# Optimization experiments

Hardware: AMD Instinct MI355X
Metric: run time of the kernel (lower is better)

The kernel has to match this reference:

```python
import jax, jax.numpy as jnp
import numpy as np

B, S, D = 2, 2048, 1024
H, DK, DV = 16, 64, 64

def setup_inputs() -> dict:
    key = jax.random.key(0)
    ks = jax.random.split(key, 5)
    scale = 1.0 / np.sqrt(D)  # xavier-ish
    return {
        "Q": jax.random.normal(ks[0], (B, S, D), dtype=jnp.float32),
        "attn_mask": jax.random.uniform(ks[1], (B, S), dtype=jnp.float32),
        "W_Q": jax.random.normal(ks[2], (H * DK, D), dtype=jnp.float32) * scale,
        "b_Q": jnp.zeros((H * DK,), dtype=jnp.float32),
        "W_K": jax.random.normal(ks[3], (H * DK, D), dtype=jnp.float32) * scale,
        "b_K": jnp.zeros((H * DK,), dtype=jnp.float32),
        "W_V": jax.random.normal(ks[4], (H * DV, D), dtype=jnp.float32) * scale,
        "b_V": jnp.zeros((H * DV,), dtype=jnp.float32),
    }

def reference(Q, attn_mask, W_Q, b_Q, W_K, b_K, W_V, b_V):
    b, s, _ = Q.shape
    # projections -> [B, H, S, d]
    q = (Q @ W_Q.T + b_Q).reshape(b, s, H, DK).transpose(0, 2, 1, 3)
    k = (Q @ W_K.T + b_K).reshape(b, s, H, DK).transpose(0, 2, 1, 3)
    v = (Q @ W_V.T + b_V).reshape(b, s, H, DV).transpose(0, 2, 1, 3)
    # exp-based attention (NOT stable softmax), multiplicative mask
    scores = jnp.einsum('bhqd,bhkd->bhqk', q, k) / np.sqrt(DK)
    scores = jnp.exp(scores)
    # mask [B, S_key] broadcast over heads and queries -> [B, 1, 1, S]
    scores = scores * attn_mask[:, None, None, :]
    attn = scores / (jnp.sum(scores, axis=-1, keepdims=True) + 1e-8)
    context = jnp.einsum('bhqk,bhkd->bhqd', attn, v)
    # [B, H, S, DV] -> [B, S, H*DV]
    return context.transpose(0, 2, 1, 3).reshape(b, s, H * DV)
```

## Files before the change

### kernel.cpp

```cpp
#include <hip/hip_runtime.h>
#include <hip/hip_bf16.h>
#include <math.h>

#define BATCH  2
#define S_LEN  2048
#define DMODEL 1024
#define NH     16
#define DHEAD  64

typedef __attribute__((ext_vector_type(8))) short bf16x8;
typedef __attribute__((ext_vector_type(4))) float f32x4;

#define MFMA16(a,b,c) __builtin_amdgcn_mfma_f32_16x16x32_bf16((a),(b),(c),0,0,0)

__device__ __forceinline__ unsigned int pkbf(float a, float b) {
    __hip_bfloat162 h = __float22bfloat162_rn(make_float2(a, b));
    union { __hip_bfloat162 h; unsigned int u; } v; v.h = h; return v.u;
}
__device__ __forceinline__ void gl2lds16(const void* g, void* l) {
    __builtin_amdgcn_global_load_lds(
        (const __attribute__((address_space(1))) void*)(g),
        (__attribute__((address_space(3))) void*)(l), 16, 0, 0);
}

__global__ __launch_bounds__(256) void cvt_bf16(
    const float* __restrict__ src, unsigned short* __restrict__ dst, int n8)
{
    int i = blockIdx.x * blockDim.x + threadIdx.x;
    if (i >= n8) return;
    float4 a = ((const float4*)src)[2*i];
    float4 b = ((const float4*)src)[2*i + 1];
    uint4 o;
    o.x = pkbf(a.x, a.y); o.y = pkbf(a.z, a.w);
    o.z = pkbf(b.x, b.y); o.w = pkbf(b.z, b.w);
    ((uint4*)dst)[i] = o;
}

__global__ __launch_bounds__(256) void proj_mfma(
    const unsigned short* __restrict__ Abf,
    const unsigned short* __restrict__ Wbf,
    const float* __restrict__ bQ, const float* __restrict__ bK,
    const float* __restrict__ bV, const float* __restrict__ mask,
    unsigned short* __restrict__ qw, unsigned short* __restrict__ kw,
    unsigned short* __restrict__ vt)
{
    __shared__ union {
        struct { unsigned short At[128*32]; unsigned short Bt[128*32]; } s;
        unsigned short Ct[128*132];
    } sm;

    const int tid  = threadIdx.x;
    const int lane = tid & 63;
    const int wv   = tid >> 6;
    const int wm   = (wv >> 1) * 64;
    const int wn   = (wv & 1) * 64;
    const int q15  = lane & 15;
    const int quad = lane >> 4;
    const int z    = blockIdx.z;
    const int n0   = blockIdx.x * 128;
    const int m0   = blockIdx.y * 128;

    const unsigned short* Wz = Wbf + (size_t)z * DMODEL * DMODEL;
    const float* bias = (z == 0) ? bQ : ((z == 1) ? bK : bV);

    f32x4 zero4 = {0.f, 0.f, 0.f, 0.f};
    f32x4 acc[4][4];
    #pragma unroll
    for (int i = 0; i < 4; ++i)
        #pragma unroll
        for (int j = 0; j < 4; ++j) acc[i][j] = zero4;

    for (int k0 = 0; k0 < DMODEL; k0 += 32) {
        __syncthreads();
        #pragma unroll
        for (int c = 0; c < 2; ++c) {
            int o   = tid * 16 + c * 4096;
            int row = o >> 6;
            int cb  = o & 63;
            gl2lds16(Abf + (size_t)(m0 + row) * DMODEL + k0 + (cb >> 1),
                     (char*)sm.s.At + o);
            gl2lds16(Wz  + (size_t)(n0 + row) * DMODEL + k0 + (cb >> 1),
                     (char*)sm.s.Bt + o);
        }
        __syncthreads();

        bf16x8 af[4], bf[4];
        #pragma unroll
        for (int i = 0; i < 4; ++i)
            af[i] = *(const bf16x8*)(sm.s.At + (wm + i*16 + q15) * 32 + quad * 8);
        #pragma unroll
        for (int j = 0; j < 4; ++j)
            bf[j] = *(const bf16x8*)(sm.s.Bt + (wn + j*16 + q15) * 32 + quad * 8);

        if (z < 2) {
            #pragma unroll
            for (int i = 0; i < 4; ++i)
                #pragma unroll
                for (int j = 0; j < 4; ++j)
                    acc[i][j] = MFMA16(bf[j], af[i], acc[i][j]);
        } else {
            #pragma unroll
            for (int i = 0; i < 4; ++i)
                #pragma unroll
                for (int j = 0; j < 4; ++j)
                    acc[i][j] = MFMA16(af[i], bf[j], acc[i][j]);
        }
    }

    __syncthreads();

    if (z < 2) {
        const float qs = (z == 0) ? 0.125f : 1.0f;
        #pragma unroll
        for (int i = 0; i < 4; ++i) {
            int ml = wm + i*16 + q15;
            #pragma unroll
            for (int j = 0; j < 4; ++j) {
                int nl = wn + j*16 + quad*4;
                float4 b4 = *(const float4*)(bias + n0 + nl);
                f32x4 v = acc[i][j];
                uint2 u;
                u.x = pkbf((v.x + b4.x)*qs, (v.y + b4.y)*qs);
                u.y = pkbf((v.z + b4.z)*qs, (v.w + b4.w)*qs);
                *(uint2*)&sm.Ct[ml*132 + nl] = u;
            }
        }
    } else {
        #pragma unroll
        for (int i = 0; i < 4; ++i) {
            int ml = wm + i*16 + quad*4;
            int sg = m0 + ml;
            int b2 = sg >> 11, s0g = sg & 2047;
            float4 mk4 = *(const float4*)(mask + (size_t)b2*S_LEN + s0g);
            #pragma unroll
            for (int j = 0; j < 4; ++j) {
                int nl = wn + j*16 + q15;
                float bv = bias[n0 + nl];
                f32x4 v = acc[i][j];
                uint2 u;
                u.x = pkbf((v.x + bv)*mk4.x, (v.y + bv)*mk4.y);
                u.y = pkbf((v.z + bv)*mk4.z, (v.w + bv)*mk4.w);
                *(uint2*)&sm.Ct[nl*132 + ml] = u;
            }
        }
    }
    __syncthreads();

    {
        int row  = tid >> 1;
        int half = (tid & 1) * 64;
        const uint4* src = (const uint4*)&sm.Ct[row*132 + half];
        unsigned short* dst;
        if (z < 2) {
            unsigned short* outp = (z == 0) ? qw : kw;
            int mg = m0 + row;  int b2 = mg >> 11, s = mg & 2047;
            int n  = n0 + half; int hh = n >> 6;
            dst = outp + (((size_t)b2*NH + hh)*S_LEN + s)*DHEAD;
        } else {
            int n  = n0 + row;  int hh = n >> 6, dv = n & 63;
            int b2 = m0 >> 11, s0 = m0 & 2047;
            dst = vt + (((size_t)b2*NH + hh)*DHEAD + dv)*S_LEN + s0 + half;
        }
        #pragma unroll
        for (int c = 0; c < 8; ++c) ((uint4*)dst)[c] = src[c];
    }
}

__global__ __launch_bounds__(256, 2) void attn_mfma(
    const unsigned short* __restrict__ qw, const unsigned short* __restrict__ kw,
    const unsigned short* __restrict__ vt, const unsigned short* __restrict__ mbf,
    float* __restrict__ out)
{
    __shared__ __align__(16) unsigned short Ks[2][64][72];
    __shared__ __align__(16) unsigned short Vs[2][64][72];
    __shared__ __align__(16) unsigned short Ms[2][72];
    __shared__ __align__(16) unsigned short P [4][32][72];

    const int tid  = threadIdx.x;
    const int lane = tid & 63;
    const int wv   = tid >> 6;
    const int q15  = lane & 15;
    const int quad = lane >> 4;
    const int q0   = blockIdx.x * 128;
    const int h    = blockIdx.y;
    const int b    = blockIdx.z;

    const size_t headoff = ((size_t)b * NH + h) * S_LEN * DHEAD;
    const unsigned short* qb = qw + headoff;
    const unsigned short* kb = kw + headoff;
    const unsigned short* vb = vt + headoff;
    const unsigned short* mb = mbf + (size_t)b * S_LEN;

    bf16x8 qf[2][2];
    #pragma unroll
    for (int qi = 0; qi < 2; ++qi) {
        const unsigned short* qr = qb + (size_t)(q0 + wv*32 + qi*16 + q15)*DHEAD;
        qf[qi][0] = *(const bf16x8*)(qr + quad*8);
        qf[qi][1] = *(const bf16x8*)(qr + 32 + quad*8);
    }

    const int srow = tid >> 3;
    const int scol = (tid & 7) * 8;

    f32x4 zero4 = {0.f, 0.f, 0.f, 0.f};
    f32x4 oacc[2][4];
    f32x4 dacc[2];
    #pragma unroll
    for (int qi = 0; qi < 2; ++qi) {
        dacc[qi] = zero4;
        #pragma unroll
        for (int nj = 0; nj < 4; ++nj) oacc[qi][nj] = zero4;
    }

    uint4 kr0, kr1, vr0, vr1, mr = {0,0,0,0};
    kr0 = *(const uint4*)(kb + (size_t)(srow)     *DHEAD + scol);
    kr1 = *(const uint4*)(kb + (size_t)(srow + 32)*DHEAD + scol);
    vr0 = *(const uint4*)(vb + (size_t)(srow)     *S_LEN + scol);
    vr1 = *(const uint4*)(vb + (size_t)(srow + 32)*S_LEN + scol);
    if (tid < 8) mr = *(const uint4*)(mb + tid*8);

    for (int t = 0; t < 32; ++t) {
        const int buf = t & 1;
        const int k0  = t * 64;
        *(uint4*)&Ks[buf][srow][scol]      = kr0;
        *(uint4*)&Ks[buf][srow + 32][scol] = kr1;
        *(uint4*)&Vs[buf][srow][scol]      = vr0;
        *(uint4*)&Vs[buf][srow + 32][scol] = vr1;
        if (tid < 8) *(uint4*)&Ms[buf][tid*8] = mr;
        const int kn = (t < 31) ? k0 + 64 : 0;
        kr0 = *(const uint4*)(kb + (size_t)(kn + srow)     *DHEAD + scol);
        kr1 = *(const uint4*)(kb + (size_t)(kn + srow + 32)*DHEAD + scol);
        vr0 = *(const uint4*)(vb + (size_t)(srow)     *S_LEN + kn + scol);
        vr1 = *(const uint4*)(vb + (size_t)(srow + 32)*S_LEN + kn + scol);
        if (tid < 8) mr = *(const uint4*)(mb + kn + tid*8);
        __syncthreads();

        f32x4 s[2][4];
        #pragma unroll
        for (int ks = 0; ks < 4; ++ks) {
            bf16x8 kf0 = *(const bf16x8*)&Ks[buf][ks*16 + q15][quad*8];
            bf16x8 kf1 = *(const bf16x8*)&Ks[buf][ks*16 + q15][32 + quad*8];
            #pragma unroll
            for (int qi = 0; qi < 2; ++qi) {
                f32x4 a = MFMA16(kf0, qf[qi][0], zero4);
                s[qi][ks] = MFMA16(kf1, qf[qi][1], a);
            }
        }
        #pragma unroll
        for (int qi = 0; qi < 2; ++qi)
            #pragma unroll
            for (int ks = 0; ks < 4; ++ks) {
                float e0 = __expf(s[qi][ks][0]);
                float e1 = __expf(s[qi][ks][1]);
                float e2 = __expf(s[qi][ks][2]);
                float e3 = __expf(s[qi][ks][3]);
                uint2 u; u.x = pkbf(e0, e1); u.y = pkbf(e2, e3);
                *(uint2*)&P[wv][qi*16 + q15][ks*16 + quad*4] = u;
            }
        bf16x8 pf[2][2];
        #pragma unroll
        for (int qi = 0; qi < 2; ++qi) {
            pf[qi][0] = *(const bf16x8*)&P[wv][qi*16 + q15][quad*8];
            pf[qi][1] = *(const bf16x8*)&P[wv][qi*16 + q15][32 + quad*8];
        }
        bf16x8 mf0 = *(const bf16x8*)&Ms[buf][quad*8];
        bf16x8 mf1 = *(const bf16x8*)&Ms[buf][32 + quad*8];
        #pragma unroll
        for (int qi = 0; qi < 2; ++qi) {
            dacc[qi] = MFMA16(pf[qi][0], mf0, dacc[qi]);
            dacc[qi] = MFMA16(pf[qi][1], mf1, dacc[qi]);
        }
        #pragma unroll
        for (int nj = 0; nj < 4; ++nj) {
            bf16x8 vf0 = *(const bf16x8*)&Vs[buf][nj*16 + q15][quad*8];
            bf16x8 vf1 = *(const bf16x8*)&Vs[buf][nj*16 + q15][32 + quad*8];
            #pragma unroll
            for (int qi = 0; qi < 2; ++qi) {
                oacc[qi][nj] = MFMA16(pf[qi][0], vf0, oacc[qi][nj]);
                oacc[qi][nj] = MFMA16(pf[qi][1], vf1, oacc[qi][nj]);
            }
        }
    }

    #pragma unroll
    for (int qi = 0; qi < 2; ++qi)
        #pragma unroll
        for (int r = 0; r < 4; ++r) {
            float inv = 1.0f / (dacc[qi][r] + 1e-8f);
            size_t row = ((size_t)b*S_LEN + q0 + wv*32 + qi*16 + quad*4 + r)*DMODEL
                       + h*DHEAD;
            #pragma unroll
            for (int nj = 0; nj < 4; ++nj)
                out[row + nj*16 + q15] = oacc[qi][nj][r] * inv;
        }
}

extern "C" void kernel_launch(void* const* d_in, const int* in_sizes, int n_in,
                              void* d_out, int out_size, void* d_ws, size_t ws_size,
                              hipStream_t stream) {
    const float* Q    = (const float*)d_in[0];
    const float* msk  = (const float*)d_in[1];
    const float* W_Q  = (const float*)d_in[2];
    const float* b_Q  = (const float*)d_in[3];
    const float* W_K  = (const float*)d_in[4];
    const float* b_K  = (const float*)d_in[5];
    const float* W_V  = (const float*)d_in[6];
    const float* b_V  = (const float*)d_in[7];
    float* out = (float*)d_out;

    unsigned short* wsu = (unsigned short*)d_ws;
    unsigned short* Qbf = wsu;
    unsigned short* Wbf = Qbf + (size_t)4096*1024;
    unsigned short* qwb = Wbf + (size_t)3*1024*1024;
    unsigned short* kwb = qwb + (size_t)4*1024*1024;
    unsigned short* vtb = kwb + (size_t)4*1024*1024;
    unsigned short* mbf = vtb + (size_t)4*1024*1024;

    cvt_bf16<<<2048, 256, 0, stream>>>(Q,   Qbf,                4096*1024/8);
    cvt_bf16<<<512,  256, 0, stream>>>(W_Q, Wbf,                1024*1024/8);
    cvt_bf16<<<512,  256, 0, stream>>>(W_K, Wbf + 1024*1024,    1024*1024/8);
    cvt_bf16<<<512,  256, 0, stream>>>(W_V, Wbf + 2*1024*1024,  1024*1024/8);
    cvt_bf16<<<2,    256, 0, stream>>>(msk, mbf,                BATCH*S_LEN/8);

    proj_mfma<<<dim3(8, 32, 3), 256, 0, stream>>>(
        Qbf, Wbf, b_Q, b_K, b_V, msk, qwb, kwb, vtb);

    attn_mfma<<<dim3(S_LEN/128, NH, BATCH), 256, 0, stream>>>(
        qwb, kwb, vtb, mbf, out);
}
```

Baseline: 195.2 us.

## Keep attention probabilities in registers, use exp2, merge conversion kernels

The attention kernel no longer writes exp-scores to an LDS P buffer and reads them back. K rows are permuted on their way into shared memory so the score MFMA output layout matches the operand layout of the PV MFMA, and the packed bf16 probabilities are built directly in registers. The Q scale now folds in log2(e) so the hardware exp2 can stand in for expf. The five bf16 conversion launches are merged into one kernel to cut launch overhead. The risk is a wrong row permutation, and slightly different rounding from exp2.

```diff
diff --git a/kernel.cpp b/kernel.cpp
--- a/kernel.cpp
+++ b/kernel.cpp
@@ -13,6 +13,9 @@
 
 #define MFMA16(a,b,c) __builtin_amdgcn_mfma_f32_16x16x32_bf16((a),(b),(c),0,0,0)
 
+#define QSCALE 0.18033688011110793f
+#define EXP2F(x) __builtin_amdgcn_exp2f(x)
+
 __device__ __forceinline__ unsigned int pkbf(float a, float b) {
     __hip_bfloat162 h = __float22bfloat162_rn(make_float2(a, b));
     union { __hip_bfloat162 h; unsigned int u; } v; v.h = h; return v.u;
@@ -23,17 +26,36 @@
         (__attribute__((address_space(3))) void*)(l), 16, 0, 0);
 }
 
-__global__ __launch_bounds__(256) void cvt_bf16(
-    const float* __restrict__ src, unsigned short* __restrict__ dst, int n8)
+__global__ __launch_bounds__(256) void cvt_all(
+    const float* __restrict__ Q,  const float* __restrict__ WQ,
+    const float* __restrict__ WK, const float* __restrict__ WV,
+    const float* __restrict__ msk,
+    unsigned short* __restrict__ Qbf, unsigned short* __restrict__ Wbf,
+    unsigned short* __restrict__ mbf)
 {
     int i = blockIdx.x * blockDim.x + threadIdx.x;
-    if (i >= n8) return;
-    float4 a = ((const float4*)src)[2*i];
-    float4 b = ((const float4*)src)[2*i + 1];
+    const float* src;
+    unsigned short* dst;
+    int off;
+    if (i < 524288) {
+        src = Q; dst = Qbf; off = i;
+    } else if (i < 917504) {
+        int j = i - 524288;
+        int which = j >> 17;
+        src = (which == 0) ? WQ : ((which == 1) ? WK : WV);
+        dst = Wbf + ((size_t)which << 20);
+        off = j & 131071;
+    } else {
+        int j = i - 917504;
+        if (j >= 512) return;
+        src = msk; dst = mbf; off = j;
+    }
+    float4 a = ((const float4*)src)[2*off];
+    float4 b = ((const float4*)src)[2*off + 1];
     uint4 o;
     o.x = pkbf(a.x, a.y); o.y = pkbf(a.z, a.w);
     o.z = pkbf(b.x, b.y); o.w = pkbf(b.z, b.w);
-    ((uint4*)dst)[i] = o;
+    ((uint4*)dst)[off] = o;
 }
 
 __global__ __launch_bounds__(256) void proj_mfma(
@@ -110,7 +132,7 @@
     __syncthreads();
 
     if (z < 2) {
-        const float qs = (z == 0) ? 0.125f : 1.0f;
+        const float qs = (z == 0) ? QSCALE : 1.0f;
         #pragma unroll
         for (int i = 0; i < 4; ++i) {
             int ml = wm + i*16 + q15;
@@ -174,7 +196,6 @@
     __shared__ __align__(16) unsigned short Ks[2][64][72];
     __shared__ __align__(16) unsigned short Vs[2][64][72];
     __shared__ __align__(16) unsigned short Ms[2][72];
-    __shared__ __align__(16) unsigned short P [4][32][72];
 
     const int tid  = threadIdx.x;
     const int lane = tid & 63;
@@ -201,6 +222,7 @@
 
     const int srow = tid >> 3;
     const int scol = (tid & 7) * 8;
+    const int prow = ((srow >> 2) & 1) * 16 + ((srow >> 3) & 3) * 4 + (srow & 3);
 
     f32x4 zero4 = {0.f, 0.f, 0.f, 0.f};
     f32x4 oacc[2][4];
@@ -222,8 +244,8 @@
     for (int t = 0; t < 32; ++t) {
         const int buf = t & 1;
         const int k0  = t * 64;
-        *(uint4*)&Ks[buf][srow][scol]      = kr0;
-        *(uint4*)&Ks[buf][srow + 32][scol] = kr1;
+        *(uint4*)&Ks[buf][prow][scol]      = kr0;
+        *(uint4*)&Ks[buf][prow + 32][scol] = kr1;
         *(uint4*)&Vs[buf][srow][scol]      = vr0;
         *(uint4*)&Vs[buf][srow + 32][scol] = vr1;
         if (tid < 8) *(uint4*)&Ms[buf][tid*8] = mr;
@@ -246,22 +268,22 @@
                 s[qi][ks] = MFMA16(kf1, qf[qi][1], a);
             }
         }
-        #pragma unroll
-        for (int qi = 0; qi < 2; ++qi)
-            #pragma unroll
-            for (int ks = 0; ks < 4; ++ks) {
-                float e0 = __expf(s[qi][ks][0]);
-                float e1 = __expf(s[qi][ks][1]);
-                float e2 = __expf(s[qi][ks][2]);
-                float e3 = __expf(s[qi][ks][3]);
-                uint2 u; u.x = pkbf(e0, e1); u.y = pkbf(e2, e3);
-                *(uint2*)&P[wv][qi*16 + q15][ks*16 + quad*4] = u;
-            }
         bf16x8 pf[2][2];
         #pragma unroll
         for (int qi = 0; qi < 2; ++qi) {
-            pf[qi][0] = *(const bf16x8*)&P[wv][qi*16 + q15][quad*8];
-            pf[qi][1] = *(const bf16x8*)&P[wv][qi*16 + q15][32 + quad*8];
+            uint4 u0, u1;
+            u0.x = pkbf(EXP2F(s[qi][0][0]), EXP2F(s[qi][0][1]));
+            u0.y = pkbf(EXP2F(s[qi][0][2]), EXP2F(s[qi][0][3]));
+            u0.z = pkbf(EXP2F(s[qi][1][0]), EXP2F(s[qi][1][1]));
+            u0.w = pkbf(EXP2F(s[qi][1][2]), EXP2F(s[qi][1][3]));
+            u1.x = pkbf(EXP2F(s[qi][2][0]), EXP2F(s[qi][2][1]));
+            u1.y = pkbf(EXP2F(s[qi][2][2]), EXP2F(s[qi][2][3]));
+            u1.z = pkbf(EXP2F(s[qi][3][0]), EXP2F(s[qi][3][1]));
+            u1.w = pkbf(EXP2F(s[qi][3][2]), EXP2F(s[qi][3][3]));
+            union { uint4 u; bf16x8 h; } c0, c1;
+            c0.u = u0; c1.u = u1;
+            pf[qi][0] = c0.h;
+            pf[qi][1] = c1.h;
         }
         bf16x8 mf0 = *(const bf16x8*)&Ms[buf][quad*8];
         bf16x8 mf1 = *(const bf16x8*)&Ms[buf][32 + quad*8];
@@ -316,11 +338,7 @@
     unsigned short* vtb = kwb + (size_t)4*1024*1024;
     unsigned short* mbf = vtb + (size_t)4*1024*1024;
 
-    cvt_bf16<<<2048, 256, 0, stream>>>(Q,   Qbf,                4096*1024/8);
-    cvt_bf16<<<512,  256, 0, stream>>>(W_Q, Wbf,                1024*1024/8);
-    cvt_bf16<<<512,  256, 0, stream>>>(W_K, Wbf + 1024*1024,    1024*1024/8);
-    cvt_bf16<<<512,  256, 0, stream>>>(W_V, Wbf + 2*1024*1024,  1024*1024/8);
-    cvt_bf16<<<2,    256, 0, stream>>>(msk, mbf,                BATCH*S_LEN/8);
+    cvt_all<<<3586, 256, 0, stream>>>(Q, W_Q, W_K, W_V, msk, Qbf, Wbf, mbf);
 
     proj_mfma<<<dim3(8, 32, 3), 256, 0, stream>>>(
         Qbf, Wbf, b_Q, b_K, b_V, msk, qwb, kwb, vtb);
```

Result: faster. 181.1 us (-7.2%).
